# Performance work log

Hardware: AMD Instinct MI355X
Metric: run time of the kernel (lower is better)

Reference implementation:

```python
import jax, jax.numpy as jnp
import numpy as np
from jax import lax

SEQ, I, H = 8192, 512, 2048  # seq_len, input_size, hidden_size


def setup_inputs() -> dict:
    key = jax.random.key(0)
    ks = jax.random.split(key, 7)
    s_ih = 1.0 / np.sqrt(I)
    s_h = 1.0 / np.sqrt(H)
    return {
        "input": jax.random.normal(ks[0], (SEQ, I), dtype=jnp.float32),
        "W_ih": jax.random.normal(ks[1], (4 * H, I), dtype=jnp.float32) * s_ih,
        "W_hh": jax.random.normal(ks[2], (4 * H, H), dtype=jnp.float32) * s_h,
        "b_ih": jax.random.normal(ks[3], (4 * H,), dtype=jnp.float32) * s_h,
        "b_hh": jax.random.normal(ks[4], (4 * H,), dtype=jnp.float32) * s_h,
        "fc_w": jax.random.normal(ks[5], (1, H), dtype=jnp.float32) * s_h,
        "fc_b": jax.random.normal(ks[6], (1,), dtype=jnp.float32) * s_h,
    }


def reference(input, W_ih, W_hh, b_ih, b_hh, fc_w, fc_b):
    # Single-layer LSTM, batch=1, PyTorch gate order (i, f, g, o).
    b = b_ih + b_hh  # [4H]
    # Precompute input projections for all timesteps in one GEMM: [SEQ, 4H]
    x_proj = input @ W_ih.T + b
    h0 = jnp.zeros((H,), dtype=input.dtype)
    c0 = jnp.zeros((H,), dtype=input.dtype)

    def step(carry, xp_t):
        h, c = carry
        gates = xp_t + h @ W_hh.T  # [4H]
        i, f, g, o = jnp.split(gates, 4)
        c_new = jax.nn.sigmoid(f) * c + jax.nn.sigmoid(i) * jnp.tanh(g)
        h_new = jax.nn.sigmoid(o) * jnp.tanh(c_new)
        return (h_new, c_new), None

    (h_last, _), _ = lax.scan(step, (h0, c0), x_proj)
    # fc1 on last hidden state -> [1, 1]
    out = h_last @ fc_w.T + fc_b
    return out.reshape(1, 1)
```

## Files before the change

kernel.cpp:

```cpp
#include <hip/hip_runtime.h>
#include <hip/hip_bf16.h>

typedef _Float16 half2_t __attribute__((ext_vector_type(2)));
typedef _Float16 half8_t __attribute__((ext_vector_type(8)));
typedef float float4_t __attribute__((ext_vector_type(4)));

#define SEQ   8192
#define ISZ   512
#define HID   2048
#define G4H   8192
#define NB    256

#if __has_builtin(__builtin_amdgcn_fdot2)
#define DOT2(a, b, c) __builtin_amdgcn_fdot2((a), (b), (c), false)
#else
static __device__ __forceinline__ float DOT2(half2_t a, half2_t b, float c) {
    return c + (float)a.x * (float)b.x + (float)a.y * (float)b.y;
}
#endif

#if __has_builtin(__builtin_amdgcn_rcpf)
#define RCP(x) __builtin_amdgcn_rcpf(x)
#else
#define RCP(x) (1.0f / (x))
#endif

static __device__ __forceinline__ unsigned long long ld_u64(const void* p) {
    return __hip_atomic_load((const unsigned long long*)p, __ATOMIC_RELAXED,
                             __HIP_MEMORY_SCOPE_AGENT);
}
static __device__ __forceinline__ void st_u64(void* p, unsigned long long v) {
    __hip_atomic_store((unsigned long long*)p, v, __ATOMIC_RELAXED,
                       __HIP_MEMORY_SCOPE_AGENT);
}

template <int CTRL>
static __device__ __forceinline__ float dpp_add(float x) {
    int v = __builtin_amdgcn_update_dpp(0, __builtin_bit_cast(int, x), CTRL, 0xF,
                                        0xF, true);
    return x + __builtin_bit_cast(float, v);
}
#define DPP_XOR1  0xB1
#define DPP_XOR2  0x4E
#define DPP_XOR4  0x141
#define DPP_XOR8  0x128

__global__ __launch_bounds__(256) void cvt_f32_f16(const float* __restrict__ in,
                                                   _Float16* __restrict__ out, int n) {
    int i = (blockIdx.x * 256 + threadIdx.x) * 4;
    if (i < n) {
        float4 v = *(const float4*)(in + i);
        out[i + 0] = (_Float16)v.x;
        out[i + 1] = (_Float16)v.y;
        out[i + 2] = (_Float16)v.z;
        out[i + 3] = (_Float16)v.w;
    }
}

__global__ __launch_bounds__(256) void init_state(unsigned long long* __restrict__ words) {
    int i = blockIdx.x * 256 + threadIdx.x;
    if (i < 4096) words[i] = 0ull;
}

__global__ __launch_bounds__(256) void gemm_xproj(const _Float16* __restrict__ A,
                                                  const _Float16* __restrict__ B,
                                                  _Float16* __restrict__ C) {
    __shared__ _Float16 As[128 * 40];
    __shared__ _Float16 Bs[128 * 40];
    const int tid = threadIdx.x;
    const int bm = blockIdx.y, bn = blockIdx.x;
    const int wave = tid >> 6, lane = tid & 63;
    const int wr = wave >> 1, wc = wave & 1;
    const int l15 = lane & 15, lq = lane >> 4;

    float4_t acc[4][4];
#pragma unroll
    for (int im = 0; im < 4; im++)
#pragma unroll
        for (int in = 0; in < 4; in++)
#pragma unroll
            for (int r = 0; r < 4; r++) acc[im][in][r] = 0.f;

    for (int kt = 0; kt < ISZ; kt += 32) {
        __syncthreads();
#pragma unroll
        for (int ld = 0; ld < 2; ld++) {
            int c = tid + ld * 256;
            int r = c >> 2, ko = (c & 3) * 8;
            uint4 av = *(const uint4*)(A + (size_t)(bm * 128 + r) * ISZ + kt + ko);
            *(uint4*)(As + r * 40 + ko) = av;
            uint4 bv = *(const uint4*)(B + (size_t)(bn * 128 + r) * ISZ + kt + ko);
            *(uint4*)(Bs + r * 40 + ko) = bv;
        }
        __syncthreads();
        half8_t af[4], bf[4];
#pragma unroll
        for (int im = 0; im < 4; im++)
            af[im] = *(half8_t*)(As + (wr * 64 + im * 16 + l15) * 40 + lq * 8);
#pragma unroll
        for (int in = 0; in < 4; in++)
            bf[in] = *(half8_t*)(Bs + (wc * 64 + in * 16 + l15) * 40 + lq * 8);
#pragma unroll
        for (int im = 0; im < 4; im++)
#pragma unroll
            for (int in = 0; in < 4; in++)
                acc[im][in] = __builtin_amdgcn_mfma_f32_16x16x32_f16(af[im], bf[in], acc[im][in], 0, 0, 0);
    }
#pragma unroll
    for (int im = 0; im < 4; im++) {
        int mg = bm * 128 + wr * 64 + im * 16 + lq * 4;
#pragma unroll
        for (int in = 0; in < 4; in++) {
            int ng = bn * 128 + wc * 64 + in * 16 + l15;
            int gate = ng >> 11;
            int e = ng & 2047;
            int col2 = (e >> 3) * 32 + ((e >> 1) & 3) * 8 + gate * 2 + (e & 1);
#pragma unroll
            for (int r = 0; r < 4; r++)
                C[(size_t)(mg + r) * G4H + col2] = (_Float16)acc[im][in][r];
        }
    }
}

__global__ __launch_bounds__(256, 1) void lstm_persist(
    const float* __restrict__ Whh,
    const float* __restrict__ b_ih, const float* __restrict__ b_hh,
    const _Float16* __restrict__ xp,
    const float* __restrict__ fcw, const float* __restrict__ fcb,
    unsigned long long* __restrict__ words,
    float* __restrict__ out) {
    const int b = blockIdx.x, tid = threadIdx.x;
    const int g = tid >> 6, lane = tid & 63;
    const int pblk = (g << 6) | ((lane + b) & 63);

    __shared__ unsigned h_lds32[2][1280];

    half2_t w[8][16];
#pragma unroll
    for (int r = 0; r < 8; r++) {
        const float* wp =
            Whh + (size_t)((r >> 1) * HID + b * 8 + 2 * g + (r & 1)) * HID + lane * 32;
#pragma unroll
        for (int i = 0; i < 16; i++) {
            float2 f = *(const float2*)(wp + i * 2);
            half2_t h2;
            h2.x = (_Float16)f.x;
            h2.y = (_Float16)f.y;
            w[r][i] = h2;
        }
    }
    float bias_r = 0.f;
    if (lane < 8) {
        int row = ((lane >> 1) & 3) * HID + b * 8 + 2 * g + (lane & 1);
        bias_r = b_ih[row] + b_hh[row];
    }
    float c_reg = 0.f;

    const int s_dw = (pblk >> 2) * 20 + (pblk & 3) * 4;
    const int xpbase = b * 32 + g * 8;

    for (int t = 0; t < SEQ; ++t) {
        const unsigned ut = (unsigned)t;
        const int par = t & 1;

        float xpv = 0.f;
        if (lane < 8) xpv = (float)xp[(size_t)t * G4H + xpbase + lane];

        const unsigned long long* wp = words + (size_t)par * 2048 + pblk * 8;
        unsigned long long v0, v1, v2, v3;
        for (;;) {
            v0 = ld_u64(wp + 0);
            v1 = ld_u64(wp + 1);
            v2 = ld_u64(wp + 2);
            v3 = ld_u64(wp + 3);
            bool ok = ((unsigned)(v0 >> 32) >= ut) && ((unsigned)(v1 >> 32) >= ut) &&
                      ((unsigned)(v2 >> 32) >= ut) && ((unsigned)(v3 >> 32) >= ut);
            if (__all(ok)) break;
            __builtin_amdgcn_s_sleep(1);
        }

        *(uint4*)&h_lds32[par][s_dw] =
            make_uint4((unsigned)v0, (unsigned)v1, (unsigned)v2, (unsigned)v3);
        __syncthreads();

        union {
            uint4 q[4];
            half2_t h2[16];
        } hu;
        const uint4* hp4 = (const uint4*)((const char*)&h_lds32[par][0] + 80 * lane);
#pragma unroll
        for (int i = 0; i < 4; i++) hu.q[i] = hp4[i];

        float acc[8];
#pragma unroll
        for (int r = 0; r < 8; r++) {
            float a = 0.f;
#pragma unroll
            for (int i = 0; i < 16; i++) a = DOT2(w[r][i], hu.h2[i], a);
            acc[r] = a;
        }
#pragma unroll
        for (int r = 0; r < 8; r++) {
            acc[r] = dpp_add<DPP_XOR1>(acc[r]);
            acc[r] = dpp_add<DPP_XOR2>(acc[r]);
            acc[r] = dpp_add<DPP_XOR4>(acc[r]);
        }
        float u;
        {
            int s = lane & 7;
            float u01 = (s & 1) ? acc[1] : acc[0];
            float u23 = (s & 1) ? acc[3] : acc[2];
            float u45 = (s & 1) ? acc[5] : acc[4];
            float u67 = (s & 1) ? acc[7] : acc[6];
            float ua = (s & 2) ? u23 : u01;
            float ub = (s & 2) ? u67 : u45;
            u = (s & 4) ? ub : ua;
        }
        u = dpp_add<DPP_XOR8>(u);
        u += __shfl_xor(u, 16, 64);
        u += __shfl_xor(u, 32, 64);
        u += bias_r + xpv;

        {
            int base = lane & 1;
            float gi = __shfl(u, base + 0, 64);
            float gf = __shfl(u, base + 2, 64);
            float gg = __shfl(u, base + 4, 64);
            float go = __shfl(u, base + 6, 64);
            float si = RCP(1.f + __expf(-gi));
            float sf = RCP(1.f + __expf(-gf));
            float so = RCP(1.f + __expf(-go));
            float tg = 1.f - 2.f * RCP(1.f + __expf(2.f * gg));
            c_reg = sf * c_reg + si * tg;
            float tc = 1.f - 2.f * RCP(1.f + __expf(2.f * c_reg));
            float h = so * tc;
            _Float16 hf = (_Float16)h;
            unsigned pk = *(unsigned short*)&hf;
            unsigned pk1 = __shfl(pk, 1, 64);
            if (lane == 0) {
                unsigned lo = pk | (pk1 << 16);
                unsigned long long wword =
                    (unsigned long long)lo | ((unsigned long long)(ut + 1) << 32);
                st_u64(words + (size_t)((t + 1) & 1) * 2048 + b * 8 + g, wword);
            }
        }
    }

    if (b == 0) {
        const int par = SEQ & 1;
        const unsigned long long* wp = words + (size_t)par * 2048 + pblk * 8;
        unsigned long long v0, v1, v2, v3;
        for (;;) {
            v0 = ld_u64(wp + 0);
            v1 = ld_u64(wp + 1);
            v2 = ld_u64(wp + 2);
            v3 = ld_u64(wp + 3);
            bool ok = ((unsigned)(v0 >> 32) >= (unsigned)SEQ) &&
                      ((unsigned)(v1 >> 32) >= (unsigned)SEQ) &&
                      ((unsigned)(v2 >> 32) >= (unsigned)SEQ) &&
                      ((unsigned)(v3 >> 32) >= (unsigned)SEQ);
            if (__all(ok)) break;
            __builtin_amdgcn_s_sleep(1);
        }
        *(uint4*)&h_lds32[par][s_dw] =
            make_uint4((unsigned)v0, (unsigned)v1, (unsigned)v2, (unsigned)v3);
        __syncthreads();
        if (g == 0) {
            union {
                uint4 q[4];
                half2_t h2[16];
            } hu;
            const uint4* hp4 = (const uint4*)((const char*)&h_lds32[par][0] + 80 * lane);
#pragma unroll
            for (int i = 0; i < 4; i++) hu.q[i] = hp4[i];
            float s = 0.f;
            const float* fw = fcw + lane * 32;
#pragma unroll
            for (int i = 0; i < 16; i++)
                s += (float)hu.h2[i].x * fw[2 * i] + (float)hu.h2[i].y * fw[2 * i + 1];
#pragma unroll
            for (int off = 1; off < 64; off <<= 1) s += __shfl_xor(s, off, 64);
            if (lane == 0) out[0] = s + fcb[0];
        }
    }
}

extern "C" void kernel_launch(void* const* d_in, const int* in_sizes, int n_in,
                              void* d_out, int out_size, void* d_ws, size_t ws_size,
                              hipStream_t stream) {
    const float* input = (const float*)d_in[0];
    const float* W_ih = (const float*)d_in[1];
    const float* W_hh = (const float*)d_in[2];
    const float* b_ih = (const float*)d_in[3];
    const float* b_hh = (const float*)d_in[4];
    const float* fc_w = (const float*)d_in[5];
    const float* fc_b = (const float*)d_in[6];
    float* out = (float*)d_out;

    char* ws = (char*)d_ws;
    _Float16* xp16 = (_Float16*)ws;
    _Float16* A16 = (_Float16*)(ws + 134217728);
    _Float16* B16 = (_Float16*)(ws + 142606336);
    unsigned long long* words = (unsigned long long*)(ws + 134217728);

    cvt_f32_f16<<<(SEQ * ISZ) / 1024, 256, 0, stream>>>(input, A16, SEQ * ISZ);
    cvt_f32_f16<<<(G4H * ISZ) / 1024, 256, 0, stream>>>(W_ih, B16, G4H * ISZ);

    dim3 gg(G4H / 128, SEQ / 128);
    gemm_xproj<<<gg, 256, 0, stream>>>(A16, B16, xp16);

    init_state<<<16, 256, 0, stream>>>(words);

    lstm_persist<<<NB, 256, 0, stream>>>(W_hh, b_ih, b_hh, xp16, fc_w, fc_b,
                                         words, out);
}
```

Before: 15.04 ms.

## Replicate hidden-state flag words across copies and use wide inline-asm polling

Each block's published h word plus step counter is now written to NREP=8 replicated copies of the buffer, and each block polls the copy selected by its index. This spreads the 256-block polling traffic over more cache lines and channels. Polling now uses two 16-byte inline-asm global loads with sc1 in place of four relaxed 64-bit atomics. Gate and neighbour exchanges use DPP shifts instead of __shfl. The cost is extra stores per step and reliance on sc1 cache semantics for coherence across CUs.

```diff
diff --git a/kernel.cpp b/kernel.cpp
--- a/kernel.cpp
+++ b/kernel.cpp
@@ -4,12 +4,14 @@
 typedef _Float16 half2_t __attribute__((ext_vector_type(2)));
 typedef _Float16 half8_t __attribute__((ext_vector_type(8)));
 typedef float float4_t __attribute__((ext_vector_type(4)));
+typedef unsigned uint4_t __attribute__((ext_vector_type(4)));
 
 #define SEQ   8192
 #define ISZ   512
 #define HID   2048
 #define G4H   8192
 #define NB    256
+#define NREP  8
 
 #if __has_builtin(__builtin_amdgcn_fdot2)
 #define DOT2(a, b, c) __builtin_amdgcn_fdot2((a), (b), (c), false)
@@ -25,13 +27,21 @@
 #define RCP(x) (1.0f / (x))
 #endif
 
-static __device__ __forceinline__ unsigned long long ld_u64(const void* p) {
-    return __hip_atomic_load((const unsigned long long*)p, __ATOMIC_RELAXED,
-                             __HIP_MEMORY_SCOPE_AGENT);
-}
 static __device__ __forceinline__ void st_u64(void* p, unsigned long long v) {
     __hip_atomic_store((unsigned long long*)p, v, __ATOMIC_RELAXED,
                        __HIP_MEMORY_SCOPE_AGENT);
+}
+
+static __device__ __forceinline__ void poll_load32(const void* p, uint4_t& a,
+                                                   uint4_t& b) {
+    unsigned long long addr = (unsigned long long)p;
+    asm volatile(
+        "global_load_dwordx4 %0, %2, off sc1\n\t"
+        "global_load_dwordx4 %1, %2, off offset:16 sc1\n\t"
+        "s_waitcnt vmcnt(0)"
+        : "=&v"(a), "=&v"(b)
+        : "v"(addr)
+        : "memory");
 }
 
 template <int CTRL>
@@ -40,10 +50,20 @@
                                         0xF, true);
     return x + __builtin_bit_cast(float, v);
 }
+template <int CTRL>
+static __device__ __forceinline__ float dpp_movf(float x) {
+    int v = __builtin_amdgcn_update_dpp(0, __builtin_bit_cast(int, x), CTRL, 0xF,
+                                        0xF, true);
+    return __builtin_bit_cast(float, v);
+}
 #define DPP_XOR1  0xB1
 #define DPP_XOR2  0x4E
 #define DPP_XOR4  0x141
 #define DPP_XOR8  0x128
+#define DPP_SHL1  0x101
+#define DPP_SHL2  0x102
+#define DPP_SHL4  0x104
+#define DPP_SHL6  0x106
 
 __global__ __launch_bounds__(256) void cvt_f32_f16(const float* __restrict__ in,
                                                    _Float16* __restrict__ out, int n) {
@@ -59,7 +79,7 @@
 
 __global__ __launch_bounds__(256) void init_state(unsigned long long* __restrict__ words) {
     int i = blockIdx.x * 256 + threadIdx.x;
-    if (i < 4096) words[i] = 0ull;
+    if (i < 2 * NREP * 2048) words[i] = 0ull;
 }
 
 __global__ __launch_bounds__(256) void gemm_xproj(const _Float16* __restrict__ A,
@@ -158,6 +178,7 @@
 
     const int s_dw = (pblk >> 2) * 20 + (pblk & 3) * 4;
     const int xpbase = b * 32 + g * 8;
+    const int rsel = b & (NREP - 1);
 
     for (int t = 0; t < SEQ; ++t) {
         const unsigned ut = (unsigned)t;
@@ -166,28 +187,26 @@
         float xpv = 0.f;
         if (lane < 8) xpv = (float)xp[(size_t)t * G4H + xpbase + lane];
 
-        const unsigned long long* wp = words + (size_t)par * 2048 + pblk * 8;
-        unsigned long long v0, v1, v2, v3;
+        const unsigned long long* wp =
+            words + ((size_t)par * NREP + rsel) * 2048 + (size_t)pblk * 8;
+        uint4_t qa, qb;
         for (;;) {
-            v0 = ld_u64(wp + 0);
-            v1 = ld_u64(wp + 1);
-            v2 = ld_u64(wp + 2);
-            v3 = ld_u64(wp + 3);
-            bool ok = ((unsigned)(v0 >> 32) >= ut) && ((unsigned)(v1 >> 32) >= ut) &&
-                      ((unsigned)(v2 >> 32) >= ut) && ((unsigned)(v3 >> 32) >= ut);
+            poll_load32(wp, qa, qb);
+            bool ok = (qa.y >= ut) && (qa.w >= ut) && (qb.y >= ut) && (qb.w >= ut);
             if (__all(ok)) break;
             __builtin_amdgcn_s_sleep(1);
         }
 
-        *(uint4*)&h_lds32[par][s_dw] =
-            make_uint4((unsigned)v0, (unsigned)v1, (unsigned)v2, (unsigned)v3);
+        uint4_t stg;
+        stg.x = qa.x; stg.y = qa.z; stg.z = qb.x; stg.w = qb.z;
+        *(uint4_t*)&h_lds32[par][s_dw] = stg;
         __syncthreads();
 
         union {
-            uint4 q[4];
+            uint4_t q[4];
             half2_t h2[16];
         } hu;
-        const uint4* hp4 = (const uint4*)((const char*)&h_lds32[par][0] + 80 * lane);
+        const uint4_t* hp4 = (const uint4_t*)((const char*)&h_lds32[par][0] + 80 * lane);
 #pragma unroll
         for (int i = 0; i < 4; i++) hu.q[i] = hp4[i];
 
@@ -222,11 +241,10 @@
         u += bias_r + xpv;
 
         {
-            int base = lane & 1;
-            float gi = __shfl(u, base + 0, 64);
-            float gf = __shfl(u, base + 2, 64);
-            float gg = __shfl(u, base + 4, 64);
-            float go = __shfl(u, base + 6, 64);
+            float gi = u;
+            float gf = dpp_movf<DPP_SHL2>(u);
+            float gg = dpp_movf<DPP_SHL4>(u);
+            float go = dpp_movf<DPP_SHL6>(u);
             float si = RCP(1.f + __expf(-gi));
             float sf = RCP(1.f + __expf(-gf));
             float so = RCP(1.f + __expf(-go));
@@ -236,41 +254,40 @@
             float h = so * tc;
             _Float16 hf = (_Float16)h;
             unsigned pk = *(unsigned short*)&hf;
-            unsigned pk1 = __shfl(pk, 1, 64);
-            if (lane == 0) {
-                unsigned lo = pk | (pk1 << 16);
-                unsigned long long wword =
-                    (unsigned long long)lo | ((unsigned long long)(ut + 1) << 32);
-                st_u64(words + (size_t)((t + 1) & 1) * 2048 + b * 8 + g, wword);
-            }
+            unsigned pk1 = (unsigned)__builtin_amdgcn_update_dpp(
+                0, (int)pk, DPP_SHL1, 0xF, 0xF, true);
+            unsigned lo = pk | (pk1 << 16);
+            unsigned lou = (unsigned)__builtin_amdgcn_readfirstlane((int)lo);
+            unsigned long long wword =
+                (unsigned long long)lou | ((unsigned long long)(ut + 1) << 32);
+            unsigned long long* wb =
+                words + (size_t)((t + 1) & 1) * (NREP * 2048) + (size_t)b * 8 + g;
+            if (lane < NREP) st_u64(wb + (size_t)lane * 2048, wword);
         }
     }
 
     if (b == 0) {
         const int par = SEQ & 1;
-        const unsigned long long* wp = words + (size_t)par * 2048 + pblk * 8;
-        unsigned long long v0, v1, v2, v3;
+        const unsigned long long* wp =
+            words + ((size_t)par * NREP + rsel) * 2048 + (size_t)pblk * 8;
+        uint4_t qa, qb;
         for (;;) {
-            v0 = ld_u64(wp + 0);
-            v1 = ld_u64(wp + 1);
-            v2 = ld_u64(wp + 2);
-            v3 = ld_u64(wp + 3);
-            bool ok = ((unsigned)(v0 >> 32) >= (unsigned)SEQ) &&
-                      ((unsigned)(v1 >> 32) >= (unsigned)SEQ) &&
-                      ((unsigned)(v2 >> 32) >= (unsigned)SEQ) &&
-                      ((unsigned)(v3 >> 32) >= (unsigned)SEQ);
+            poll_load32(wp, qa, qb);
+            bool ok = (qa.y >= (unsigned)SEQ) && (qa.w >= (unsigned)SEQ) &&
+                      (qb.y >= (unsigned)SEQ) && (qb.w >= (unsigned)SEQ);
             if (__all(ok)) break;
             __builtin_amdgcn_s_sleep(1);
         }
-        *(uint4*)&h_lds32[par][s_dw] =
-            make_uint4((unsigned)v0, (unsigned)v1, (unsigned)v2, (unsigned)v3);
+        uint4_t stg;
+        stg.x = qa.x; stg.y = qa.z; stg.z = qb.x; stg.w = qb.z;
+        *(uint4_t*)&h_lds32[par][s_dw] = stg;
         __syncthreads();
         if (g == 0) {
             union {
-                uint4 q[4];
+                uint4_t q[4];
                 half2_t h2[16];
             } hu;
-            const uint4* hp4 = (const uint4*)((const char*)&h_lds32[par][0] + 80 * lane);
+            const uint4_t* hp4 = (const uint4_t*)((const char*)&h_lds32[par][0] + 80 * lane);
 #pragma unroll
             for (int i = 0; i < 4; i++) hu.q[i] = hp4[i];
             float s = 0.f;
@@ -309,7 +326,7 @@
     dim3 gg(G4H / 128, SEQ / 128);
     gemm_xproj<<<gg, 256, 0, stream>>>(A16, B16, xp16);
 
-    init_state<<<16, 256, 0, stream>>>(words);
+    init_state<<<(2 * NREP * 2048) / 256, 256, 0, stream>>>(words);
 
     lstm_persist<<<NB, 256, 0, stream>>>(W_hh, b_ih, b_hh, xp16, fc_w, fc_b,
                                          words, out);
```

Result: faster. 12.90 ms (-14.3%).
